# Kernel tuning notes

Measured on AMD Instinct MI355X. Metric: run time of the kernel, lower is better.

## Reference

```python
import jax, jax.numpy as jnp
import numpy as np
from jax.experimental.ode import odeint

RTOL, ATOL = 1e-4, 1e-5


def setup_inputs() -> dict:
    key = jax.random.key(0)
    ks = jax.random.split(key, 8)
    B, T = 16384, 256

    def lin(k, fan_in, fan_out):
        return jax.random.normal(k, (fan_in, fan_out), jnp.float32) / np.sqrt(fan_in)

    return {
        "x": jax.random.normal(ks[0], (B, T, 9), jnp.float32),
        "We1": lin(ks[1], 9, 64), "be1": jnp.zeros((64,), jnp.float32),
        "We2": lin(ks[2], 64, 64), "be2": jnp.zeros((64,), jnp.float32),
        "We3": lin(ks[3], 64, 2), "be3": jnp.zeros((2,), jnp.float32),
        "Wo1": lin(ks[4], 2, 32), "bo1": jnp.zeros((32,), jnp.float32),
        "Wo2": lin(ks[5], 32, 2), "bo2": jnp.zeros((2,), jnp.float32),
        "Wd": lin(ks[6], 2, 3), "bd": jnp.zeros((3,), jnp.float32),
    }


def reference(x, We1, be1, We2, be2, We3, be3, Wo1, bo1, Wo2, bo2, Wd, bd):
    B, T, C = x.shape
    # Encoder: 9 -> 64 -> 64 -> 2 (ReLU) on the first time-step only
    h = jax.nn.relu(x[:, 0, :] @ We1 + be1)
    h = jax.nn.relu(h @ We2 + be2)
    z0 = h @ We3 + be3                      # (B, 2)

    t_span = jnp.linspace(0.0, 1.0, T)      # default t_span in forward()

    # Autonomous tanh-MLP vector field: 2 -> 32 -> 2
    def vf(z, t, Wo1, bo1, Wo2, bo2):
        return jnp.tanh(z @ Wo1 + bo1) @ Wo2 + bo2

    # Adaptive dopri5, matching torchdiffeq's odeint(method='dopri5')
    z_traj = odeint(vf, z0, t_span, Wo1, bo1, Wo2, bo2, rtol=RTOL, atol=ATOL)  # (T, B, 2)

    x_hat = z_traj @ Wd + bd                # (T, B, 3) linear decoder
    return (z0, z_traj, x_hat)
```

## Files before the change

### kernel.cpp

```cpp
#include <hip/hip_runtime.h>


constexpr int   BATCH = 16384;
constexpr int   NSEG  = 6;
constexpr float DT    = 1.0f / (float)NSEG;
constexpr float DT2   = DT * 0.5f;
constexpr float DT6   = DT / 6.0f;
constexpr float SCALE = 2.8853900817779268f;
constexpr float K255  = (float)NSEG / 255.0f;

__device__ __forceinline__ float fast_exp2(float x) {
#if __has_builtin(__builtin_amdgcn_exp2f)
  return __builtin_amdgcn_exp2f(x);
#else
  return exp2f(x);
#endif
}

__device__ __forceinline__ float fast_rcp(float x) {
#if __has_builtin(__builtin_amdgcn_rcpf)
  return __builtin_amdgcn_rcpf(x);
#else
  return 1.0f / x;
#endif
}

template<int CTRL>
__device__ __forceinline__ float dpp_add(float v) {
  int sw = __builtin_amdgcn_update_dpp(0, __float_as_int(v), CTRL, 0xF, 0xF, true);
  return v + __int_as_float(sw);
}

__device__ __forceinline__ float allred16(float v) {
  v = dpp_add<0xB1>(v);
  v = dpp_add<0x4E>(v);
  v = dpp_add<0x141>(v);
  v = dpp_add<0x140>(v);
  return v;
}

__global__ __launch_bounds__(256) void gait_all(
    const float* __restrict__ x,
    const float* __restrict__ We1, const float* __restrict__ be1,
    const float* __restrict__ We2, const float* __restrict__ be2,
    const float* __restrict__ We3, const float* __restrict__ be3,
    const float* __restrict__ Wo1, const float* __restrict__ bo1,
    const float* __restrict__ Wo2, const float* __restrict__ bo2,
    const float* __restrict__ Wd,  const float* __restrict__ bd,
    float* __restrict__ out)
{
  const int tid = threadIdx.x;
  const int t   = blockIdx.x * 256 + tid;
  const int b   = t >> 4;
  const int sub = t & 15;
  const int sg  = tid >> 4;

  __shared__ float4 bndl[NSEG + 1][16];
  __shared__ float  h1l[16][64];

  const float* xb = x + (size_t)b * 2304;
  float xv[9];
#pragma unroll
  for (int i = 0; i < 9; ++i) xv[i] = xb[i];

  const int c0 = sub * 4;
#pragma unroll
  for (int ii = 0; ii < 4; ++ii) {
    const int i = c0 + ii;
    float h = be1[i];
#pragma unroll
    for (int j = 0; j < 9; ++j) h = fmaf(xv[j], We1[j*64 + i], h);
    h1l[sg][i] = fmaxf(h, 0.0f);
  }
  __syncthreads();

  float s0 = be2[c0+0], s1 = be2[c0+1], s2 = be2[c0+2], s3 = be2[c0+3];
#pragma unroll 4
  for (int i = 0; i < 64; i += 4) {
    const float4 h4 = *reinterpret_cast<const float4*>(&h1l[sg][i]);
    const float* w2r0 = We2 + (i    )*64 + c0;
    const float* w2r1 = We2 + (i + 1)*64 + c0;
    const float* w2r2 = We2 + (i + 2)*64 + c0;
    const float* w2r3 = We2 + (i + 3)*64 + c0;
    s0 = fmaf(h4.x, w2r0[0], s0); s1 = fmaf(h4.x, w2r0[1], s1);
    s2 = fmaf(h4.x, w2r0[2], s2); s3 = fmaf(h4.x, w2r0[3], s3);
    s0 = fmaf(h4.y, w2r1[0], s0); s1 = fmaf(h4.y, w2r1[1], s1);
    s2 = fmaf(h4.y, w2r1[2], s2); s3 = fmaf(h4.y, w2r1[3], s3);
    s0 = fmaf(h4.z, w2r2[0], s0); s1 = fmaf(h4.z, w2r2[1], s1);
    s2 = fmaf(h4.z, w2r2[2], s2); s3 = fmaf(h4.z, w2r2[3], s3);
    s0 = fmaf(h4.w, w2r3[0], s0); s1 = fmaf(h4.w, w2r3[1], s1);
    s2 = fmaf(h4.w, w2r3[2], s2); s3 = fmaf(h4.w, w2r3[3], s3);
  }
  s0 = fmaxf(s0, 0.0f); s1 = fmaxf(s1, 0.0f);
  s2 = fmaxf(s2, 0.0f); s3 = fmaxf(s3, 0.0f);
  float z0a = fmaf(s0, We3[(c0+0)*2+0], fmaf(s1, We3[(c0+1)*2+0],
              fmaf(s2, We3[(c0+2)*2+0],      s3 * We3[(c0+3)*2+0])));
  float z0b = fmaf(s0, We3[(c0+0)*2+1], fmaf(s1, We3[(c0+1)*2+1],
              fmaf(s2, We3[(c0+2)*2+1],      s3 * We3[(c0+3)*2+1])));
  z0a = allred16(z0a) + be3[0];
  z0b = allred16(z0b) + be3[1];

  if (sub == 5) {
    float2 v; v.x = z0a; v.y = z0b;
    *reinterpret_cast<float2*>(out + (size_t)b * 2) = v;
  }

  float w1a[2], w1b[2], b1s[2], w2a[2], w2b[2];
  const int u0 = sub * 2;
#pragma unroll
  for (int q = 0; q < 2; ++q) {
    w1a[q] = Wo1[      u0 + q] * SCALE;
    w1b[q] = Wo1[32 +  u0 + q] * SCALE;
    b1s[q] = bo1[      u0 + q] * SCALE;
    w2a[q] = Wo2[(u0 + q)*2 + 0];
    w2b[q] = Wo2[(u0 + q)*2 + 1];
  }
  const float a0i = (sub == 0) ? bo2[0] : 0.0f;
  const float a1i = (sub == 0) ? bo2[1] : 0.0f;

  auto vf = [&](float za, float zb, float& o0, float& o1) {
    float a0 = a0i, a1 = a1i;
#pragma unroll
    for (int q = 0; q < 2; ++q) {
      float u  = fmaf(za, w1a[q], fmaf(zb, w1b[q], b1s[q]));
      float e  = fast_exp2(u);
      float rr = fast_rcp(e + 1.0f);
      float th = fmaf(-2.0f, rr, 1.0f);
      a0 = fmaf(th, w2a[q], a0);
      a1 = fmaf(th, w2b[q], a1);
    }
    o0 = allred16(a0);
    o1 = allred16(a1);
  };

  const float wd0 = Wd[0], wd1 = Wd[1], wd2 = Wd[2];
  const float wd3 = Wd[3], wd4 = Wd[4], wd5 = Wd[5];
  const float bd0 = bd[0], bd1 = bd[1], bd2 = bd[2];

  const int es     = tid & 15;
  const int empart = tid >> 4;
  const int gb     = blockIdx.x * 16 + es;

  float* __restrict__ zt = out + 32768;
  float* __restrict__ xh = out + 32768 + 8388608;

  auto emit_seg = [&](int seg) {
    const int m0s   = (seg == 0) ? 0 : (255 * seg) / NSEG + 1;
    const int mlast = (255 * (seg + 1)) / NSEG;
    const float4 p0 = bndl[seg][es];
    const float4 p1 = bndl[seg + 1][es];
    const float fadt  = DT * p0.z, fbdt  = DT * p0.w;
    const float fnadt = DT * p1.z, fnbdt = DT * p1.w;
    const float da = p1.x - p0.x, db = p1.y - p0.y;
    const float c2a = fmaf(3.f, da, -fmaf(2.f, fadt, fnadt));
    const float c3a = fmaf(-2.f, da, fadt + fnadt);
    const float c2b = fmaf(3.f, db, -fmaf(2.f, fbdt, fnbdt));
    const float c3b = fmaf(-2.f, db, fbdt + fnbdt);
    const float segneg = -(float)seg;
#pragma unroll
    for (int sl = 0; sl < 3; ++sl) {
      const int m = m0s + empart + (sl << 4);
      if (m <= mlast) {
        const float th = fmaf((float)m, K255, segneg);
        const float va = fmaf(fmaf(fmaf(c3a, th, c2a), th, fadt), th, p0.x);
        const float vb = fmaf(fmaf(fmaf(c3b, th, c2b), th, fbdt), th, p0.y);
        float2 zv; zv.x = va; zv.y = vb;
        *reinterpret_cast<float2*>(zt + ((size_t)m << 15) + 2 * gb) = zv;
        float* q = xh + (size_t)m * 49152 + 3 * gb;
        q[0] = fmaf(va, wd0, fmaf(vb, wd3, bd0));
        q[1] = fmaf(va, wd1, fmaf(vb, wd4, bd1));
        q[2] = fmaf(va, wd2, fmaf(vb, wd5, bd2));
      }
    }
  };

  float za = z0a, zb = z0b;
  float fa, fb;
  vf(za, zb, fa, fb);

  const bool storer = (sub == 0);

#pragma unroll 1
  for (int k = 0; k < NSEG; ++k) {
    if (storer) { float4 v; v.x = za; v.y = zb; v.z = fa; v.w = fb;
                  bndl[k][sg] = v; }
    __syncthreads();

    float k2a, k2b, k3a, k3b, k4a, k4b, fna, fnb;
    vf(fmaf(DT2, fa,  za), fmaf(DT2, fb,  zb), k2a, k2b);
    if (k >= 1) emit_seg(k - 1);
    vf(fmaf(DT2, k2a, za), fmaf(DT2, k2b, zb), k3a, k3b);
    vf(fmaf(DT,  k3a, za), fmaf(DT,  k3b, zb), k4a, k4b);
    float zna = fmaf(DT6, fa + k4a + 2.0f*(k2a + k3a), za);
    float znb = fmaf(DT6, fb + k4b + 2.0f*(k2b + k3b), zb);
    vf(zna, znb, fna, fnb);
    za = zna; zb = znb; fa = fna; fb = fnb;
  }
  if (storer) { float4 v; v.x = za; v.y = zb; v.z = fa; v.w = fb;
                bndl[NSEG][sg] = v; }
  __syncthreads();
  emit_seg(NSEG - 1);
}

extern "C" void kernel_launch(void* const* d_in, const int* in_sizes, int n_in,
                              void* d_out, int out_size, void* d_ws, size_t ws_size,
                              hipStream_t stream)
{
  const float* x   = (const float*)d_in[0];
  const float* We1 = (const float*)d_in[1];
  const float* be1 = (const float*)d_in[2];
  const float* We2 = (const float*)d_in[3];
  const float* be2 = (const float*)d_in[4];
  const float* We3 = (const float*)d_in[5];
  const float* be3 = (const float*)d_in[6];
  const float* Wo1 = (const float*)d_in[7];
  const float* bo1 = (const float*)d_in[8];
  const float* Wo2 = (const float*)d_in[9];
  const float* bo2 = (const float*)d_in[10];
  const float* Wd  = (const float*)d_in[11];
  const float* bd  = (const float*)d_in[12];

  dim3 grid(BATCH * 16 / 256), block(256);
  gait_all<<<grid, block, 0, stream>>>(x, We1, be1, We2, be2, We3, be3,
                                       Wo1, bo1, Wo2, bo2, Wd, bd,
                                       (float*)d_out);
}
```

Baseline: 27.31 us.

## Split block into integrator and emitter warp groups for producer-consumer overlap

Doubles the block to 512 threads. The first 256 threads run the encoder and the RK4 integration and publish segment boundaries to shared memory, while the second 256 threads only interpolate and write the trajectory and decoded outputs. Previously the same threads interleaved vf evaluations with emit stores. The split lets the stores of segment k-1 overlap with the integration of segment k, at the cost of one extra loop iteration of barriers and more threads per block.

```diff
diff --git a/kernel.cpp b/kernel.cpp
--- a/kernel.cpp
+++ b/kernel.cpp
@@ -39,7 +39,7 @@
   return v;
 }
 
-__global__ __launch_bounds__(256) void gait_all(
+__global__ __launch_bounds__(512) void gait_all(
     const float* __restrict__ x,
     const float* __restrict__ We1, const float* __restrict__ be1,
     const float* __restrict__ We2, const float* __restrict__ be2,
@@ -49,80 +49,96 @@
     const float* __restrict__ Wd,  const float* __restrict__ bd,
     float* __restrict__ out)
 {
-  const int tid = threadIdx.x;
-  const int t   = blockIdx.x * 256 + tid;
-  const int b   = t >> 4;
-  const int sub = t & 15;
-  const int sg  = tid >> 4;
+  const int tid    = threadIdx.x;
+  const bool is_int = (tid < 256);
 
   __shared__ float4 bndl[NSEG + 1][16];
   __shared__ float  h1l[16][64];
 
-  const float* xb = x + (size_t)b * 2304;
-  float xv[9];
-#pragma unroll
-  for (int i = 0; i < 9; ++i) xv[i] = xb[i];
-
-  const int c0 = sub * 4;
-#pragma unroll
-  for (int ii = 0; ii < 4; ++ii) {
-    const int i = c0 + ii;
-    float h = be1[i];
-#pragma unroll
-    for (int j = 0; j < 9; ++j) h = fmaf(xv[j], We1[j*64 + i], h);
-    h1l[sg][i] = fmaxf(h, 0.0f);
+  const int sub = tid & 15;
+  const int sg  = (tid >> 4) & 15;
+  const int b   = blockIdx.x * 16 + sg;
+  const int c0  = sub * 4;
+
+  if (is_int) {
+    const float* xb = x + (size_t)b * 2304;
+    float xv[9];
+#pragma unroll
+    for (int i = 0; i < 9; ++i) xv[i] = xb[i];
+#pragma unroll
+    for (int ii = 0; ii < 4; ++ii) {
+      const int i = c0 + ii;
+      float h = be1[i];
+#pragma unroll
+      for (int j = 0; j < 9; ++j) h = fmaf(xv[j], We1[j*64 + i], h);
+      h1l[sg][i] = fmaxf(h, 0.0f);
+    }
   }
   __syncthreads();
 
-  float s0 = be2[c0+0], s1 = be2[c0+1], s2 = be2[c0+2], s3 = be2[c0+3];
+  float za = 0.f, zb = 0.f, fa = 0.f, fb = 0.f;
+  float w1a[2] = {0,0}, w1b[2] = {0,0}, b1s[2] = {0,0};
+  float w2a[2] = {0,0}, w2b[2] = {0,0};
+  float a0i = 0.f, a1i = 0.f;
+  float wd0=0,wd1=0,wd2=0,wd3=0,wd4=0,wd5=0,bd0=0,bd1=0,bd2=0;
+  int   gb = 0;
+
+  if (is_int) {
+    float s0 = be2[c0+0], s1 = be2[c0+1], s2 = be2[c0+2], s3 = be2[c0+3];
 #pragma unroll 4
-  for (int i = 0; i < 64; i += 4) {
-    const float4 h4 = *reinterpret_cast<const float4*>(&h1l[sg][i]);
-    const float* w2r0 = We2 + (i    )*64 + c0;
-    const float* w2r1 = We2 + (i + 1)*64 + c0;
-    const float* w2r2 = We2 + (i + 2)*64 + c0;
-    const float* w2r3 = We2 + (i + 3)*64 + c0;
-    s0 = fmaf(h4.x, w2r0[0], s0); s1 = fmaf(h4.x, w2r0[1], s1);
-    s2 = fmaf(h4.x, w2r0[2], s2); s3 = fmaf(h4.x, w2r0[3], s3);
-    s0 = fmaf(h4.y, w2r1[0], s0); s1 = fmaf(h4.y, w2r1[1], s1);
-    s2 = fmaf(h4.y, w2r1[2], s2); s3 = fmaf(h4.y, w2r1[3], s3);
-    s0 = fmaf(h4.z, w2r2[0], s0); s1 = fmaf(h4.z, w2r2[1], s1);
-    s2 = fmaf(h4.z, w2r2[2], s2); s3 = fmaf(h4.z, w2r2[3], s3);
-    s0 = fmaf(h4.w, w2r3[0], s0); s1 = fmaf(h4.w, w2r3[1], s1);
-    s2 = fmaf(h4.w, w2r3[2], s2); s3 = fmaf(h4.w, w2r3[3], s3);
+    for (int i = 0; i < 64; i += 4) {
+      const float4 h4 = *reinterpret_cast<const float4*>(&h1l[sg][i]);
+      const float* w2r0 = We2 + (i    )*64 + c0;
+      const float* w2r1 = We2 + (i + 1)*64 + c0;
+      const float* w2r2 = We2 + (i + 2)*64 + c0;
+      const float* w2r3 = We2 + (i + 3)*64 + c0;
+      s0 = fmaf(h4.x, w2r0[0], s0); s1 = fmaf(h4.x, w2r0[1], s1);
+      s2 = fmaf(h4.x, w2r0[2], s2); s3 = fmaf(h4.x, w2r0[3], s3);
+      s0 = fmaf(h4.y, w2r1[0], s0); s1 = fmaf(h4.y, w2r1[1], s1);
+      s2 = fmaf(h4.y, w2r1[2], s2); s3 = fmaf(h4.y, w2r1[3], s3);
+      s0 = fmaf(h4.z, w2r2[0], s0); s1 = fmaf(h4.z, w2r2[1], s1);
+      s2 = fmaf(h4.z, w2r2[2], s2); s3 = fmaf(h4.z, w2r2[3], s3);
+      s0 = fmaf(h4.w, w2r3[0], s0); s1 = fmaf(h4.w, w2r3[1], s1);
+      s2 = fmaf(h4.w, w2r3[2], s2); s3 = fmaf(h4.w, w2r3[3], s3);
+    }
+    s0 = fmaxf(s0, 0.0f); s1 = fmaxf(s1, 0.0f);
+    s2 = fmaxf(s2, 0.0f); s3 = fmaxf(s3, 0.0f);
+    float z0a = fmaf(s0, We3[(c0+0)*2+0], fmaf(s1, We3[(c0+1)*2+0],
+                fmaf(s2, We3[(c0+2)*2+0],      s3 * We3[(c0+3)*2+0])));
+    float z0b = fmaf(s0, We3[(c0+0)*2+1], fmaf(s1, We3[(c0+1)*2+1],
+                fmaf(s2, We3[(c0+2)*2+1],      s3 * We3[(c0+3)*2+1])));
+    z0a = allred16(z0a) + be3[0];
+    z0b = allred16(z0b) + be3[1];
+
+    if (sub == 5) {
+      float2 v; v.x = z0a; v.y = z0b;
+      *reinterpret_cast<float2*>(out + (size_t)b * 2) = v;
+    }
+
+    const int u0 = sub * 2;
+#pragma unroll
+    for (int q = 0; q < 2; ++q) {
+      w1a[q] = Wo1[      u0 + q] * SCALE;
+      w1b[q] = Wo1[32 +  u0 + q] * SCALE;
+      b1s[q] = bo1[      u0 + q] * SCALE;
+      w2a[q] = Wo2[(u0 + q)*2 + 0];
+      w2b[q] = Wo2[(u0 + q)*2 + 1];
+    }
+    a0i = (sub == 0) ? bo2[0] : 0.0f;
+    a1i = (sub == 0) ? bo2[1] : 0.0f;
+    za = z0a; zb = z0b;
+  } else {
+    wd0 = Wd[0]; wd1 = Wd[1]; wd2 = Wd[2];
+    wd3 = Wd[3]; wd4 = Wd[4]; wd5 = Wd[5];
+    bd0 = bd[0]; bd1 = bd[1]; bd2 = bd[2];
+    gb  = blockIdx.x * 16 + sub;
   }
-  s0 = fmaxf(s0, 0.0f); s1 = fmaxf(s1, 0.0f);
-  s2 = fmaxf(s2, 0.0f); s3 = fmaxf(s3, 0.0f);
-  float z0a = fmaf(s0, We3[(c0+0)*2+0], fmaf(s1, We3[(c0+1)*2+0],
-              fmaf(s2, We3[(c0+2)*2+0],      s3 * We3[(c0+3)*2+0])));
-  float z0b = fmaf(s0, We3[(c0+0)*2+1], fmaf(s1, We3[(c0+1)*2+1],
-              fmaf(s2, We3[(c0+2)*2+1],      s3 * We3[(c0+3)*2+1])));
-  z0a = allred16(z0a) + be3[0];
-  z0b = allred16(z0b) + be3[1];
-
-  if (sub == 5) {
-    float2 v; v.x = z0a; v.y = z0b;
-    *reinterpret_cast<float2*>(out + (size_t)b * 2) = v;
-  }
-
-  float w1a[2], w1b[2], b1s[2], w2a[2], w2b[2];
-  const int u0 = sub * 2;
-#pragma unroll
-  for (int q = 0; q < 2; ++q) {
-    w1a[q] = Wo1[      u0 + q] * SCALE;
-    w1b[q] = Wo1[32 +  u0 + q] * SCALE;
-    b1s[q] = bo1[      u0 + q] * SCALE;
-    w2a[q] = Wo2[(u0 + q)*2 + 0];
-    w2b[q] = Wo2[(u0 + q)*2 + 1];
-  }
-  const float a0i = (sub == 0) ? bo2[0] : 0.0f;
-  const float a1i = (sub == 0) ? bo2[1] : 0.0f;
-
-  auto vf = [&](float za, float zb, float& o0, float& o1) {
+
+  auto vf = [&](float pza, float pzb, float& o0, float& o1) {
     float a0 = a0i, a1 = a1i;
 #pragma unroll
     for (int q = 0; q < 2; ++q) {
-      float u  = fmaf(za, w1a[q], fmaf(zb, w1b[q], b1s[q]));
+      float u  = fmaf(pza, w1a[q], fmaf(pzb, w1b[q], b1s[q]));
       float e  = fast_exp2(u);
       float rr = fast_rcp(e + 1.0f);
       float th = fmaf(-2.0f, rr, 1.0f);
@@ -133,22 +149,14 @@
     o1 = allred16(a1);
   };
 
-  const float wd0 = Wd[0], wd1 = Wd[1], wd2 = Wd[2];
-  const float wd3 = Wd[3], wd4 = Wd[4], wd5 = Wd[5];
-  const float bd0 = bd[0], bd1 = bd[1], bd2 = bd[2];
-
-  const int es     = tid & 15;
-  const int empart = tid >> 4;
-  const int gb     = blockIdx.x * 16 + es;
-
   float* __restrict__ zt = out + 32768;
   float* __restrict__ xh = out + 32768 + 8388608;
 
   auto emit_seg = [&](int seg) {
     const int m0s   = (seg == 0) ? 0 : (255 * seg) / NSEG + 1;
     const int mlast = (255 * (seg + 1)) / NSEG;
-    const float4 p0 = bndl[seg][es];
-    const float4 p1 = bndl[seg + 1][es];
+    const float4 p0 = bndl[seg][sub];
+    const float4 p1 = bndl[seg + 1][sub];
     const float fadt  = DT * p0.z, fbdt  = DT * p0.w;
     const float fnadt = DT * p1.z, fnbdt = DT * p1.w;
     const float da = p1.x - p0.x, db = p1.y - p0.y;
@@ -159,7 +167,7 @@
     const float segneg = -(float)seg;
 #pragma unroll
     for (int sl = 0; sl < 3; ++sl) {
-      const int m = m0s + empart + (sl << 4);
+      const int m = m0s + sg + (sl << 4);
       if (m <= mlast) {
         const float th = fmaf((float)m, K255, segneg);
         const float va = fmaf(fmaf(fmaf(c3a, th, c2a), th, fadt), th, p0.x);
@@ -174,32 +182,31 @@
     }
   };
 
-  float za = z0a, zb = z0b;
-  float fa, fb;
-  vf(za, zb, fa, fb);
-
-  const bool storer = (sub == 0);
+  if (is_int) vf(za, zb, fa, fb);
+
+  const bool storer = is_int && (sub == 0);
 
 #pragma unroll 1
-  for (int k = 0; k < NSEG; ++k) {
+  for (int k = 0; k <= NSEG; ++k) {
     if (storer) { float4 v; v.x = za; v.y = zb; v.z = fa; v.w = fb;
                   bndl[k][sg] = v; }
     __syncthreads();
 
-    float k2a, k2b, k3a, k3b, k4a, k4b, fna, fnb;
-    vf(fmaf(DT2, fa,  za), fmaf(DT2, fb,  zb), k2a, k2b);
-    if (k >= 1) emit_seg(k - 1);
-    vf(fmaf(DT2, k2a, za), fmaf(DT2, k2b, zb), k3a, k3b);
-    vf(fmaf(DT,  k3a, za), fmaf(DT,  k3b, zb), k4a, k4b);
-    float zna = fmaf(DT6, fa + k4a + 2.0f*(k2a + k3a), za);
-    float znb = fmaf(DT6, fb + k4b + 2.0f*(k2b + k3b), zb);
-    vf(zna, znb, fna, fnb);
-    za = zna; zb = znb; fa = fna; fb = fnb;
+    if (is_int) {
+      if (k < NSEG) {
+        float k2a, k2b, k3a, k3b, k4a, k4b, fna, fnb;
+        vf(fmaf(DT2, fa,  za), fmaf(DT2, fb,  zb), k2a, k2b);
+        vf(fmaf(DT2, k2a, za), fmaf(DT2, k2b, zb), k3a, k3b);
+        vf(fmaf(DT,  k3a, za), fmaf(DT,  k3b, zb), k4a, k4b);
+        float zna = fmaf(DT6, fa + k4a + 2.0f*(k2a + k3a), za);
+        float znb = fmaf(DT6, fb + k4b + 2.0f*(k2b + k3b), zb);
+        vf(zna, znb, fna, fnb);
+        za = zna; zb = znb; fa = fna; fb = fnb;
+      }
+    } else if (k >= 1) {
+      emit_seg(k - 1);
+    }
   }
-  if (storer) { float4 v; v.x = za; v.y = zb; v.z = fa; v.w = fb;
-                bndl[NSEG][sg] = v; }
-  __syncthreads();
-  emit_seg(NSEG - 1);
 }
 
 extern "C" void kernel_launch(void* const* d_in, const int* in_sizes, int n_in,
@@ -220,7 +227,7 @@
   const float* Wd  = (const float*)d_in[11];
   const float* bd  = (const float*)d_in[12];
 
-  dim3 grid(BATCH * 16 / 256), block(256);
+  dim3 grid(BATCH / 16), block(512);
   gait_all<<<grid, block, 0, stream>>>(x, We1, be1, We2, be2, We3, be3,
                                        Wo1, bo1, Wo2, bo2, Wd, bd,
                                        (float*)d_out);
```

New measurement: 27.05 us (median of 2 runs). Within noise of the previous version (-0.9%).
